# Kernel optimization log

Hardware: AMD Instinct MI355X
Metric: run time of the kernel (lower is better)

Reference implementation:

```python
import jax, jax.numpy as jnp
import numpy as np

K = 3            # TAGConv default number of hops
NUM_GRAPHS = 128 # graphs in the batch (for global_add_pool)


def _gcn_norm(src, dst, n):
    # PyG gcn_norm (symmetric, no self-loops): w_e = d[src]^-1/2 * d[dst]^-1/2
    deg = jnp.zeros((n,), jnp.float32).at[dst].add(1.0)
    dinv = jnp.where(deg > 0, jax.lax.rsqrt(deg), 0.0)
    return dinv[src] * dinv[dst]


def _tagconv(x, src, dst, wn, W, b):
    # out = sum_{k=0..K} (norm_adj^k x) @ W[k] + b
    n = x.shape[0]
    h = x
    out = h @ W[0]
    for k in range(1, K + 1):
        h = jax.ops.segment_sum(h[src] * wn[:, None], dst, num_segments=n)
        out = out + h @ W[k]
    return out + b


def setup_inputs() -> dict:
    key = jax.random.key(0)
    ks = jax.random.split(key, 8)
    N, E, D, H = 50000, 800000, 64, 64
    x = jax.random.normal(ks[0], (N, D), jnp.float32)
    edge_index = jax.random.randint(ks[1], (2, E), 0, N, dtype=jnp.int32)
    batch_ids = jnp.sort(jax.random.randint(ks[2], (N,), 0, NUM_GRAPHS, dtype=jnp.int32))
    def glorot(k, sh):
        return jax.random.normal(k, sh, jnp.float32) / np.float32(np.sqrt(sh[-2]))
    W0 = glorot(ks[3], (K + 1, D, H)); b0 = jnp.zeros((H,), jnp.float32)
    W1 = glorot(ks[4], (K + 1, H, H)); b1 = jnp.zeros((H,), jnp.float32)
    alpha0 = jnp.full((1,), 0.25, jnp.float32)  # PReLU default init
    alpha1 = jnp.full((1,), 0.25, jnp.float32)
    Wout = glorot(ks[5], (H, 1)); bout = jnp.zeros((1,), jnp.float32)
    return dict(x=x, edge_index=edge_index, batch_ids=batch_ids,
                W0=W0, b0=b0, W1=W1, b1=b1,
                alpha0=alpha0, alpha1=alpha1, Wout=Wout, bout=bout)


def reference(x, edge_index, batch_ids, W0, b0, W1, b1, alpha0, alpha1, Wout, bout):
    src, dst = edge_index[0], edge_index[1]
    wn = _gcn_norm(src, dst, x.shape[0])
    # layer 0: TAGConv -> (dropout=identity in eval) -> PReLU
    h = _tagconv(x, src, dst, wn, W0, b0)
    h = jnp.where(h >= 0, h, alpha0 * h)
    # layer 1
    h = _tagconv(h, src, dst, wn, W1, b1)
    h = jnp.where(h >= 0, h, alpha1 * h)
    # global_add_pool over graphs, then linear critic head
    g = jax.ops.segment_sum(h, batch_ids, num_segments=NUM_GRAPHS)  # [G, H]
    return g @ Wout + bout  # [G, 1]
```

## Files before the change

### kernel.cpp

```cpp
#include <hip/hip_runtime.h>
#include <hip/hip_bf16.h>
#include <hip/hip_fp16.h>

#define D 64
#define GRAPHS 128

using bf16x8 = __attribute__((ext_vector_type(8))) short;
using f32x4  = __attribute__((ext_vector_type(4))) float;


__device__ __forceinline__ float bf2f(unsigned short u) {
    return __uint_as_float(((unsigned)u) << 16);
}
__device__ __forceinline__ unsigned short f2bf(float f) {
    unsigned u = __float_as_uint(f);
    unsigned r = (u + 0x7FFFu + ((u >> 16) & 1u)) >> 16;
    return (unsigned short)r;
}


__global__ void deg_prep_kernel(const int* __restrict__ dst, int* __restrict__ deg,
                                int* __restrict__ pos, int E, int EB,
                                const float* __restrict__ W0, const float* __restrict__ W1,
                                unsigned short* __restrict__ WF0, unsigned short* __restrict__ WF1,
                                const float* __restrict__ x, unsigned short* __restrict__ H, int total) {
    int b = blockIdx.x;
    if (b < EB) {
        int e = b * 256 + threadIdx.x;
        if (e < E) pos[e] = atomicAdd(&deg[dst[e]], 1);
    } else if (b < EB + 128) {
        int idx = (b - EB) * 256 + threadIdx.x;
        int i = idx & 16383;
        int j = i & 7, lane = (i >> 3) & 63, ct = (i >> 9) & 3, kt = i >> 11;
        int n = ct * 16 + (lane & 15);
        int k = kt * 32 + (lane >> 4) * 8 + j;
        if (idx < 16384) WF0[i] = f2bf(W0[k * 64 + n]);
        else             WF1[i] = f2bf(W1[k * 64 + n]);
    } else {
        int i = (b - EB - 128) * 256 + threadIdx.x;
        if (i < total) {
            int n = i >> 6, f = i & 63;
            H[(size_t)n * 256 + f] = f2bf(x[i]);
        }
    }
}


__global__ void scan_all_kernel(const int* __restrict__ deg, float* __restrict__ dinv,
                                int* __restrict__ pdeg, int* __restrict__ rowstart,
                                unsigned int* __restrict__ ep, int* __restrict__ total, int N) {
    __shared__ int s[256];
    __shared__ int base_sh;
    int i = blockIdx.x * 256 + threadIdx.x;
    int d = 0, p = 0;
    if (i < N) {
        d = deg[i];
        dinv[i] = d > 0 ? rsqrtf((float)d) : 0.0f;
        p = (d + 7) & ~7;
        pdeg[i] = p;
    }
    s[threadIdx.x] = p;
    __syncthreads();
    for (int st = 1; st < 256; st <<= 1) {
        int add = (threadIdx.x >= st) ? s[threadIdx.x - st] : 0;
        __syncthreads();
        s[threadIdx.x] += add;
        __syncthreads();
    }
    if (threadIdx.x == 255) base_sh = atomicAdd(total, s[255]);
    __syncthreads();
    if (i < N) {
        int excl = base_sh + s[threadIdx.x] - p;
        rowstart[i] = excl;
        for (int q = excl + d; q < excl + p; ++q) ep[q] = 0u;
    }
}


__global__ void scatter_kernel(const int* __restrict__ src, const int* __restrict__ dst,
                               const int* __restrict__ pos, const float* __restrict__ dinv,
                               const int* __restrict__ rowstart, unsigned int* __restrict__ ep, int E) {
    int e = blockIdx.x * blockDim.x + threadIdx.x;
    if (e < E) {
        int d = dst[e], s = src[e];
        unsigned short wu = __half_as_ushort(__float2half(dinv[s]));
        ep[rowstart[d] + pos[e]] = (unsigned)s | ((unsigned)wu << 16);
    }
}


#define GROWS 8

__global__ __launch_bounds__(512, 8)
void gather_kernel(const unsigned short* __restrict__ in,
                   unsigned short* __restrict__ out,
                   const int* __restrict__ rowstart, const int* __restrict__ pdeg,
                   const float* __restrict__ dinv, const unsigned int* __restrict__ ep, int N) {
    int wid = blockIdx.x * GROWS + (threadIdx.x >> 6);
    if (wid >= N) return;
    int lane = threadIdx.x & 63;
    int g  = lane >> 4;
    int fl = (lane & 15) * 4;

    int start = __builtin_amdgcn_readfirstlane(rowstart[wid]);
    int cnt   = __builtin_amdgcn_readfirstlane(pdeg[wid]);
    float dd  = dinv[wid];

    float a0 = 0.f, a1 = 0.f, a2 = 0.f, a3 = 0.f;
    float b0 = 0.f, b1 = 0.f, b2 = 0.f, b3 = 0.f;
    unsigned eA = 0, eB = 0;
    if (cnt > 0) { eA = ep[start + g]; eB = ep[start + 4 + g]; }
    for (int i = 0; i < cnt; i += 8) {
        unsigned cA = eA, cB = eB;
        if (i + 8 < cnt) { eA = ep[start + i + 8 + g]; eB = ep[start + i + 12 + g]; }
        ushort4 rA = *(const ushort4*)(in + (size_t)(cA & 0xFFFFu) * 256 + fl);
        ushort4 rB = *(const ushort4*)(in + (size_t)(cB & 0xFFFFu) * 256 + fl);
        float wA = __half2float(__ushort_as_half((unsigned short)(cA >> 16)));
        float wB = __half2float(__ushort_as_half((unsigned short)(cB >> 16)));
        a0 = fmaf(wA, bf2f(rA.x), a0);
        a1 = fmaf(wA, bf2f(rA.y), a1);
        a2 = fmaf(wA, bf2f(rA.z), a2);
        a3 = fmaf(wA, bf2f(rA.w), a3);
        b0 = fmaf(wB, bf2f(rB.x), b0);
        b1 = fmaf(wB, bf2f(rB.y), b1);
        b2 = fmaf(wB, bf2f(rB.z), b2);
        b3 = fmaf(wB, bf2f(rB.w), b3);
    }
    a0 += b0; a1 += b1; a2 += b2; a3 += b3;
    a0 += __shfl_xor(a0, 16, 64); a0 += __shfl_xor(a0, 32, 64);
    a1 += __shfl_xor(a1, 16, 64); a1 += __shfl_xor(a1, 32, 64);
    a2 += __shfl_xor(a2, 16, 64); a2 += __shfl_xor(a2, 32, 64);
    a3 += __shfl_xor(a3, 16, 64); a3 += __shfl_xor(a3, 32, 64);
    if (g == 0) {
        ushort4 pk;
        pk.x = f2bf(a0 * dd); pk.y = f2bf(a1 * dd); pk.z = f2bf(a2 * dd); pk.w = f2bf(a3 * dd);
        *(ushort4*)(out + (size_t)wid * 256 + fl) = pk;
    }
}


template<int MODE>
__global__ __launch_bounds__(256, 4)
void tag_gemm_kernel(const unsigned short* __restrict__ H,
                     const unsigned short* __restrict__ Wfrag,
                     const float* __restrict__ bias, const float* __restrict__ alpha,
                     const float* __restrict__ Wout, const int* __restrict__ batch,
                     const float* __restrict__ bout,
                     unsigned short* __restrict__ H2, float* __restrict__ outp, int N) {
    __shared__ float bins[GRAPHS];
    if (MODE == 3) {
        if (threadIdx.x < GRAPHS) bins[threadIdx.x] = 0.0f;
        __syncthreads();
    }
    if (MODE == 2) {
        if (blockIdx.x == 0 && threadIdx.x < GRAPHS) outp[threadIdx.x] = bout[0];
    }

    int w = threadIdx.x >> 6, lane = threadIdx.x & 63;
    int m = lane & 15, quad = lane >> 4;
    int rowbase = blockIdx.x * 64 + w * 16;
    int arow = rowbase + m;
    size_t aoff = (size_t)min(arow, N - 1) * 256 + quad * 8;

    f32x4 acc0 = {0.f, 0.f, 0.f, 0.f}, acc1 = acc0, acc2 = acc0, acc3 = acc0;
#pragma unroll
    for (int kt = 0; kt < 8; ++kt) {
        bf16x8 A = *(const bf16x8*)(H + aoff + kt * 32);
        const unsigned short* wf = Wfrag + ((size_t)(kt * 4) * 64 + lane) * 8;
        bf16x8 B0 = *(const bf16x8*)(wf + 0 * 64 * 8);
        bf16x8 B1 = *(const bf16x8*)(wf + 1 * 64 * 8);
        bf16x8 B2 = *(const bf16x8*)(wf + 2 * 64 * 8);
        bf16x8 B3 = *(const bf16x8*)(wf + 3 * 64 * 8);
        acc0 = __builtin_amdgcn_mfma_f32_16x16x32_bf16(A, B0, acc0, 0, 0, 0);
        acc1 = __builtin_amdgcn_mfma_f32_16x16x32_bf16(A, B1, acc1, 0, 0, 0);
        acc2 = __builtin_amdgcn_mfma_f32_16x16x32_bf16(A, B2, acc2, 0, 0, 0);
        acc3 = __builtin_amdgcn_mfma_f32_16x16x32_bf16(A, B3, acc3, 0, 0, 0);
    }

    float al = alpha[0];
    f32x4 accs[4] = {acc0, acc1, acc2, acc3};
    if (MODE == 2) {
#pragma unroll
        for (int ct = 0; ct < 4; ++ct) {
            int col = ct * 16 + m;
            float b = bias[col];
#pragma unroll
            for (int r = 0; r < 4; ++r) {
                int row = rowbase + quad * 4 + r;
                if (row < N) {
                    float v = accs[ct][r] + b;
                    v = v >= 0.f ? v : al * v;
                    H2[(size_t)row * 256 + col] = f2bf(v);
                }
            }
        }
    } else {
        float rv0 = 0.f, rv1 = 0.f, rv2 = 0.f, rv3 = 0.f;
#pragma unroll
        for (int ct = 0; ct < 4; ++ct) {
            int col = ct * 16 + m;
            float b = bias[col], wo = Wout[col];
            float v;
            v = accs[ct][0] + b; v = v >= 0.f ? v : al * v; rv0 = fmaf(v, wo, rv0);
            v = accs[ct][1] + b; v = v >= 0.f ? v : al * v; rv1 = fmaf(v, wo, rv1);
            v = accs[ct][2] + b; v = v >= 0.f ? v : al * v; rv2 = fmaf(v, wo, rv2);
            v = accs[ct][3] + b; v = v >= 0.f ? v : al * v; rv3 = fmaf(v, wo, rv3);
        }
        float rv[4] = {rv0, rv1, rv2, rv3};
#pragma unroll
        for (int r = 0; r < 4; ++r) {
            float v = rv[r];
            v += __shfl_xor(v, 8, 16);
            v += __shfl_xor(v, 4, 16);
            v += __shfl_xor(v, 2, 16);
            v += __shfl_xor(v, 1, 16);
            int row = rowbase + quad * 4 + r;
            if (m == 0 && row < N) atomicAdd(&bins[batch[row]], v);
        }
        __syncthreads();
        if (threadIdx.x < GRAPHS) {
            float bv = bins[threadIdx.x];
            if (bv != 0.0f) atomicAdd(&outp[threadIdx.x], bv);
        }
    }
}

extern "C" void kernel_launch(void* const* d_in, const int* in_sizes, int n_in,
                              void* d_out, int out_size, void* d_ws, size_t ws_size,
                              hipStream_t stream) {
    const float* x     = (const float*)d_in[0];
    const int*   ei    = (const int*)d_in[1];
    const int*   batch = (const int*)d_in[2];
    const float* W0    = (const float*)d_in[3];
    const float* b0    = (const float*)d_in[4];
    const float* W1    = (const float*)d_in[5];
    const float* b1    = (const float*)d_in[6];
    const float* a0    = (const float*)d_in[7];
    const float* a1    = (const float*)d_in[8];
    const float* Wout  = (const float*)d_in[9];
    const float* bout  = (const float*)d_in[10];

    const int N = in_sizes[0] / D;
    const int E = in_sizes[1] / 2;
    const int* src = ei;
    const int* dst = ei + E;

    size_t off = 0;
    auto alloc = [&](size_t bytes) -> void* {
        void* p = (char*)d_ws + off;
        off = (off + bytes + 255) & ~(size_t)255;
        return p;
    };
    const int NB = (N + 255) / 256;
    int*   deg      = (int*)alloc((size_t)(N + 1) * 4);
    int*   pdeg     = (int*)alloc((size_t)N * 4);
    int*   rowstart = (int*)alloc((size_t)N * 4);
    float* dinv     = (float*)alloc((size_t)N * 4);
    int*   pos      = (int*)alloc((size_t)E * 4);
    unsigned int* epack = (unsigned int*)alloc(((size_t)E + 8ull * N) * 4);
    unsigned short* HA = (unsigned short*)alloc((size_t)N * 256 * 2);
    unsigned short* HB = (unsigned short*)alloc((size_t)N * 256 * 2);
    unsigned short* WF0 = (unsigned short*)alloc(16384 * 2);
    unsigned short* WF1 = (unsigned short*)alloc(16384 * 2);

    const int EB = (E + 255) / 256;
    const int NT = (N * D + 255) / 256;
    const int NG = (N + GROWS - 1) / GROWS;
    const int NM = (N + 63) / 64;

    hipMemsetAsync(deg, 0, (size_t)(N + 1) * 4, stream);
    deg_prep_kernel<<<EB + 128 + NT, 256, 0, stream>>>(dst, deg, pos, E, EB,
                                                       W0, W1, WF0, WF1, x, HA, N * D);
    scan_all_kernel<<<NB, 256, 0, stream>>>(deg, dinv, pdeg, rowstart, epack, deg + N, N);
    scatter_kernel<<<EB, 256, 0, stream>>>(src, dst, pos, dinv, rowstart, epack, E);

    gather_kernel<<<NG, 512, 0, stream>>>(HA + 0 * 64, HA + 1 * 64, rowstart, pdeg, dinv, epack, N);
    gather_kernel<<<NG, 512, 0, stream>>>(HA + 1 * 64, HA + 2 * 64, rowstart, pdeg, dinv, epack, N);
    gather_kernel<<<NG, 512, 0, stream>>>(HA + 2 * 64, HA + 3 * 64, rowstart, pdeg, dinv, epack, N);
    tag_gemm_kernel<2><<<NM, 256, 0, stream>>>(HA, WF0, b0, a0, nullptr, nullptr, bout,
                                               HB, (float*)d_out, N);

    gather_kernel<<<NG, 512, 0, stream>>>(HB + 0 * 64, HB + 1 * 64, rowstart, pdeg, dinv, epack, N);
    gather_kernel<<<NG, 512, 0, stream>>>(HB + 1 * 64, HB + 2 * 64, rowstart, pdeg, dinv, epack, N);
    gather_kernel<<<NG, 512, 0, stream>>>(HB + 2 * 64, HB + 3 * 64, rowstart, pdeg, dinv, epack, N);
    tag_gemm_kernel<3><<<NM, 256, 0, stream>>>(HB, WF1, b1, a1, Wout, batch, bout,
                                               nullptr, (float*)d_out, N);
}
```

Baseline: 283.4 us.

## Vectorize CSR build, use cursor atomics, and deepen gather prefetch pipeline

The degree count and scatter now handle four edges per thread with int4 loads. Scatter claims slots through an atomic cursor per destination, which removes the stored per-edge position array. The x-to-bf16 conversion uses float4 loads and 16-byte packed stores. The gather loop now prefetches the next feature rows one iteration ahead and the edge entries two iterations ahead, to hide memory latency. This costs more registers and gives a nondeterministic edge order within each row, which changes the float summation order.

```diff
diff --git a/kernel.cpp b/kernel.cpp
--- a/kernel.cpp
+++ b/kernel.cpp
@@ -20,16 +20,24 @@
 
 
 __global__ void deg_prep_kernel(const int* __restrict__ dst, int* __restrict__ deg,
-                                int* __restrict__ pos, int E, int EB,
+                                int E, int EB4,
                                 const float* __restrict__ W0, const float* __restrict__ W1,
                                 unsigned short* __restrict__ WF0, unsigned short* __restrict__ WF1,
-                                const float* __restrict__ x, unsigned short* __restrict__ H, int total) {
+                                const float* __restrict__ x, unsigned short* __restrict__ H, int NH) {
     int b = blockIdx.x;
-    if (b < EB) {
-        int e = b * 256 + threadIdx.x;
-        if (e < E) pos[e] = atomicAdd(&deg[dst[e]], 1);
-    } else if (b < EB + 128) {
-        int idx = (b - EB) * 256 + threadIdx.x;
+    if (b < EB4) {
+        int e0 = (b * 256 + threadIdx.x) * 4;
+        if (e0 + 4 <= E) {
+            int4 d4 = *(const int4*)(dst + e0);
+            atomicAdd(&deg[d4.x], 1);
+            atomicAdd(&deg[d4.y], 1);
+            atomicAdd(&deg[d4.z], 1);
+            atomicAdd(&deg[d4.w], 1);
+        } else {
+            for (int e = e0; e < E; ++e) atomicAdd(&deg[dst[e]], 1);
+        }
+    } else if (b < EB4 + 128) {
+        int idx = (b - EB4) * 256 + threadIdx.x;
         int i = idx & 16383;
         int j = i & 7, lane = (i >> 3) & 63, ct = (i >> 9) & 3, kt = i >> 11;
         int n = ct * 16 + (lane & 15);
@@ -37,10 +45,15 @@
         if (idx < 16384) WF0[i] = f2bf(W0[k * 64 + n]);
         else             WF1[i] = f2bf(W1[k * 64 + n]);
     } else {
-        int i = (b - EB - 128) * 256 + threadIdx.x;
-        if (i < total) {
-            int n = i >> 6, f = i & 63;
-            H[(size_t)n * 256 + f] = f2bf(x[i]);
+        int i = (b - EB4 - 128) * 256 + threadIdx.x;
+        if (i < NH) {
+            int n = i >> 3, f = (i & 7) * 8;
+            float4 x0 = *(const float4*)(x + (size_t)n * 64 + f);
+            float4 x1 = *(const float4*)(x + (size_t)n * 64 + f + 4);
+            bf16x8 pk;
+            pk[0] = f2bf(x0.x); pk[1] = f2bf(x0.y); pk[2] = f2bf(x0.z); pk[3] = f2bf(x0.w);
+            pk[4] = f2bf(x1.x); pk[5] = f2bf(x1.y); pk[6] = f2bf(x1.z); pk[7] = f2bf(x1.w);
+            *(bf16x8*)(H + (size_t)n * 256 + f) = pk;
         }
     }
 }
@@ -48,6 +61,7 @@
 
 __global__ void scan_all_kernel(const int* __restrict__ deg, float* __restrict__ dinv,
                                 int* __restrict__ pdeg, int* __restrict__ rowstart,
+                                int* __restrict__ cursor,
                                 unsigned int* __restrict__ ep, int* __restrict__ total, int N) {
     __shared__ int s[256];
     __shared__ int base_sh;
@@ -72,19 +86,34 @@
     if (i < N) {
         int excl = base_sh + s[threadIdx.x] - p;
         rowstart[i] = excl;
+        cursor[i] = excl;
         for (int q = excl + d; q < excl + p; ++q) ep[q] = 0u;
     }
 }
 
 
 __global__ void scatter_kernel(const int* __restrict__ src, const int* __restrict__ dst,
-                               const int* __restrict__ pos, const float* __restrict__ dinv,
-                               const int* __restrict__ rowstart, unsigned int* __restrict__ ep, int E) {
-    int e = blockIdx.x * blockDim.x + threadIdx.x;
-    if (e < E) {
-        int d = dst[e], s = src[e];
-        unsigned short wu = __half_as_ushort(__float2half(dinv[s]));
-        ep[rowstart[d] + pos[e]] = (unsigned)s | ((unsigned)wu << 16);
+                               const float* __restrict__ dinv, int* __restrict__ cursor,
+                               unsigned int* __restrict__ ep, int E) {
+    int e0 = (blockIdx.x * 256 + threadIdx.x) * 4;
+    if (e0 + 4 <= E) {
+        int4 s4 = *(const int4*)(src + e0);
+        int4 d4 = *(const int4*)(dst + e0);
+        float v0 = dinv[s4.x], v1 = dinv[s4.y], v2 = dinv[s4.z], v3 = dinv[s4.w];
+        int p0 = atomicAdd(&cursor[d4.x], 1);
+        int p1 = atomicAdd(&cursor[d4.y], 1);
+        int p2 = atomicAdd(&cursor[d4.z], 1);
+        int p3 = atomicAdd(&cursor[d4.w], 1);
+        ep[p0] = (unsigned)s4.x | ((unsigned)__half_as_ushort(__float2half(v0)) << 16);
+        ep[p1] = (unsigned)s4.y | ((unsigned)__half_as_ushort(__float2half(v1)) << 16);
+        ep[p2] = (unsigned)s4.z | ((unsigned)__half_as_ushort(__float2half(v2)) << 16);
+        ep[p3] = (unsigned)s4.w | ((unsigned)__half_as_ushort(__float2half(v3)) << 16);
+    } else {
+        for (int e = e0; e < E; ++e) {
+            int dd = dst[e], ss = src[e];
+            int p = atomicAdd(&cursor[dd], 1);
+            ep[p] = (unsigned)ss | ((unsigned)__half_as_ushort(__float2half(dinv[ss])) << 16);
+        }
     }
 }
 
@@ -109,14 +138,24 @@
     float a0 = 0.f, a1 = 0.f, a2 = 0.f, a3 = 0.f;
     float b0 = 0.f, b1 = 0.f, b2 = 0.f, b3 = 0.f;
     unsigned eA = 0, eB = 0;
-    if (cnt > 0) { eA = ep[start + g]; eB = ep[start + 4 + g]; }
+    unsigned fA = 0, fB = 0;
+    ushort4 rA = {0, 0, 0, 0}, rB = {0, 0, 0, 0};
+    if (cnt > 0) {
+        eA = ep[start + g]; eB = ep[start + 4 + g];
+        if (cnt > 8) { fA = ep[start + 8 + g]; fB = ep[start + 12 + g]; }
+        rA = *(const ushort4*)(in + (size_t)(eA & 0xFFFFu) * 256 + fl);
+        rB = *(const ushort4*)(in + (size_t)(eB & 0xFFFFu) * 256 + fl);
+    }
     for (int i = 0; i < cnt; i += 8) {
-        unsigned cA = eA, cB = eB;
-        if (i + 8 < cnt) { eA = ep[start + i + 8 + g]; eB = ep[start + i + 12 + g]; }
-        ushort4 rA = *(const ushort4*)(in + (size_t)(cA & 0xFFFFu) * 256 + fl);
-        ushort4 rB = *(const ushort4*)(in + (size_t)(cB & 0xFFFFu) * 256 + fl);
-        float wA = __half2float(__ushort_as_half((unsigned short)(cA >> 16)));
-        float wB = __half2float(__ushort_as_half((unsigned short)(cB >> 16)));
+        ushort4 nA = rA, nB = rB;
+        unsigned gA = fA, gB = fB;
+        if (i + 8 < cnt) {
+            nA = *(const ushort4*)(in + (size_t)(fA & 0xFFFFu) * 256 + fl);
+            nB = *(const ushort4*)(in + (size_t)(fB & 0xFFFFu) * 256 + fl);
+            if (i + 16 < cnt) { fA = ep[start + i + 16 + g]; fB = ep[start + i + 20 + g]; }
+        }
+        float wA = __half2float(__ushort_as_half((unsigned short)(eA >> 16)));
+        float wB = __half2float(__ushort_as_half((unsigned short)(eB >> 16)));
         a0 = fmaf(wA, bf2f(rA.x), a0);
         a1 = fmaf(wA, bf2f(rA.y), a1);
         a2 = fmaf(wA, bf2f(rA.z), a2);
@@ -125,6 +164,7 @@
         b1 = fmaf(wB, bf2f(rB.y), b1);
         b2 = fmaf(wB, bf2f(rB.z), b2);
         b3 = fmaf(wB, bf2f(rB.w), b3);
+        rA = nA; rB = nB; eA = gA; eB = gB;
     }
     a0 += b0; a1 += b1; a2 += b2; a3 += b3;
     a0 += __shfl_xor(a0, 16, 64); a0 += __shfl_xor(a0, 32, 64);
@@ -255,24 +295,24 @@
     int*   deg      = (int*)alloc((size_t)(N + 1) * 4);
     int*   pdeg     = (int*)alloc((size_t)N * 4);
     int*   rowstart = (int*)alloc((size_t)N * 4);
+    int*   cursor   = (int*)alloc((size_t)N * 4);
     float* dinv     = (float*)alloc((size_t)N * 4);
-    int*   pos      = (int*)alloc((size_t)E * 4);
     unsigned int* epack = (unsigned int*)alloc(((size_t)E + 8ull * N) * 4);
     unsigned short* HA = (unsigned short*)alloc((size_t)N * 256 * 2);
     unsigned short* HB = (unsigned short*)alloc((size_t)N * 256 * 2);
     unsigned short* WF0 = (unsigned short*)alloc(16384 * 2);
     unsigned short* WF1 = (unsigned short*)alloc(16384 * 2);
 
-    const int EB = (E + 255) / 256;
-    const int NT = (N * D + 255) / 256;
+    const int EB4 = (E + 1023) / 1024;
+    const int NXH = (N * 8 + 255) / 256;
     const int NG = (N + GROWS - 1) / GROWS;
     const int NM = (N + 63) / 64;
 
     hipMemsetAsync(deg, 0, (size_t)(N + 1) * 4, stream);
-    deg_prep_kernel<<<EB + 128 + NT, 256, 0, stream>>>(dst, deg, pos, E, EB,
-                                                       W0, W1, WF0, WF1, x, HA, N * D);
-    scan_all_kernel<<<NB, 256, 0, stream>>>(deg, dinv, pdeg, rowstart, epack, deg + N, N);
-    scatter_kernel<<<EB, 256, 0, stream>>>(src, dst, pos, dinv, rowstart, epack, E);
+    deg_prep_kernel<<<EB4 + 128 + NXH, 256, 0, stream>>>(dst, deg, E, EB4,
+                                                         W0, W1, WF0, WF1, x, HA, N * 8);
+    scan_all_kernel<<<NB, 256, 0, stream>>>(deg, dinv, pdeg, rowstart, cursor, epack, deg + N, N);
+    scatter_kernel<<<EB4, 256, 0, stream>>>(src, dst, dinv, cursor, epack, E);
 
     gather_kernel<<<NG, 512, 0, stream>>>(HA + 0 * 64, HA + 1 * 64, rowstart, pdeg, dinv, epack, N);
     gather_kernel<<<NG, 512, 0, stream>>>(HA + 1 * 64, HA + 2 * 64, rowstart, pdeg, dinv, epack, N);
```

New measurement: 324.4 us. +14.5%, slower.
